# Performance work log

Measured on AMD Instinct MI355X. Metric: run time of the kernel, lower is better.

## Reference

```python
import jax, jax.numpy as jnp
import numpy as np

RATE = 0.2  # sparsification keep-rate from forward: sparse(x, 0.2)


def sparse_mask(x, rate):
    # Per-sample top-k over flattened NxN adjacency, scatter a 0/1 mask, multiply.
    b, n, _ = x.shape
    k = int(n * n * rate)
    flat = x.reshape(b, -1)
    _, idx = jax.lax.top_k(flat, k)  # [b, k]
    mask = jnp.zeros_like(flat).at[jnp.arange(b)[:, None], idx].set(1.0)
    return x * mask.reshape(b, n, n)


def gcn_layer(X, A, W, b):
    # Dense-batched equivalent of PyG GCNConv on dense_to_sparse(A) edges:
    # add self-loops (weight 1), symmetric-normalize by weighted degree,
    # aggregate source->target (row->col) messages of X @ W.
    n = A.shape[-1]
    Ah = A + jnp.eye(n, dtype=A.dtype)          # [B,N,N]
    deg = Ah.sum(axis=-2)                        # weighted in-degree (col sum), [B,N]
    dinv = jnp.where(deg > 0, 1.0 / jnp.sqrt(deg), 0.0)
    An = dinv[:, :, None] * Ah * dinv[:, None, :]  # norm_ij = d_i^-1/2 A_ij d_j^-1/2
    XW = X @ W                                     # [B,N,H]
    # out_j = sum_i An_ij * XW_i  (message flows row i -> col j)
    return jnp.einsum('bij,bih->bjh', An, XW) + b


def setup_inputs() -> dict:
    key = jax.random.key(0)
    ks = jax.random.split(key, 6)
    B, N, H = 1024, 200, 128
    return {
        "x": jax.random.uniform(ks[0], (B, N, N), jnp.float32),
        "adj": jax.random.uniform(ks[1], (B, N, N), jnp.float32),
        "W1": jax.random.normal(ks[2], (N, H), jnp.float32) * 0.05,
        "b1": jnp.zeros((H,), jnp.float32),
        "W2": jax.random.normal(ks[3], (H, H), jnp.float32) * 0.05,
        "b2": jnp.zeros((H,), jnp.float32),
    }


def reference(x, adj, W1, b1, W2, b2):
    # NOTE: the original forward immediately overwrites `adj` with sparse(x, 0.2).
    A = sparse_mask(x, RATE)
    h = jax.nn.relu(gcn_layer(x, A, W1, b1))  # GCNConv(200,128) + ReLU
    h = gcn_layer(h, A, W2, b2)                # GCNConv(128,128)
    return h.mean(axis=-2)                     # mean over nodes -> [B, 128]
```

## Files before the change

kernel.cpp:

```cpp
#include <hip/hip_runtime.h>

#define NB 1024
#define NNODE 200
#define NN2 40000
#define HD 128
#define KTOP 8000
#define NCH 7
#define NJT 13
#define XBS 232
#define A2S 40

#define WLO_BITS 0x3F47AE14u
#define WHI_BITS 0x3F51EB85u
#define CCAP 3072
#define C2CAP 64

typedef __attribute__((ext_vector_type(8))) short short8;
typedef __attribute__((ext_vector_type(4))) float f32x4;

__device__ __forceinline__ unsigned short f2bf(float f) {
  unsigned u = __float_as_uint(f);
  u = u + 0x7FFFu + ((u >> 16) & 1u);
  return (unsigned short)(u >> 16);
}

__device__ __forceinline__ float maskv(float v, int idx, unsigned vt, int it) {
  unsigned b = __float_as_uint(v);
  return (b > vt || (b == vt && idx <= it)) ? v : 0.0f;
}

__global__ void k_weights(const float* __restrict__ W1, unsigned short* __restrict__ wf) {
  int t = blockIdx.x * 256 + threadIdx.x;
  if (t >= NCH * 8 * 64) return;
  int lane = t & 63;
  int ht = (t >> 6) & 7;
  int ks = t >> 9;
  int c = lane & 15, q = lane >> 4;
  int h = ht * 16 + c;
  unsigned short v[8];
#pragma unroll
  for (int j = 0; j < 8; ++j) {
    int k = ks * 32 + q * 8 + j;
    v[j] = f2bf((k < NNODE) ? W1[k * HD + h] : 0.0f);
  }
  uint4 u;
  u.x = (unsigned)v[0] | ((unsigned)v[1] << 16);
  u.y = (unsigned)v[2] | ((unsigned)v[3] << 16);
  u.z = (unsigned)v[4] | ((unsigned)v[5] << 16);
  u.w = (unsigned)v[6] | ((unsigned)v[7] << 16);
  ((uint4*)wf)[t] = u;
}

__global__ __launch_bounds__(512) void k_prep(const float* __restrict__ x,
                                              unsigned* __restrict__ vtit,
                                              float* __restrict__ dinv_g) {
  __shared__ union {
    struct { unsigned cb[CCAP]; int ci[CCAP]; } w;
    unsigned hist[4096];
  } u;
  __shared__ unsigned sub[1024];
  __shared__ unsigned csum[512];
  __shared__ float degf[NNODE];
  __shared__ unsigned c2b[C2CAP];
  __shared__ int c2i[C2CAP];
  __shared__ int sc[4];
  __shared__ int cnt, cnt2, nhi_s, fbflag;
  __shared__ unsigned svt;
  __shared__ int sit;

  const int s = blockIdx.x, tid = threadIdx.x;
  const float* xp = x + (size_t)s * NN2;
  const float4* xp4 = (const float4*)xp;

  if (tid < NNODE) degf[tid] = 0.0f;
  if (tid == 0) { cnt = 0; cnt2 = 0; nhi_s = 0; fbflag = 0; }
  __syncthreads();

  int nhi = 0;
  for (int e = tid; e < NN2 / 4; e += 512) {
    float4 f = xp4[e];
    int base = e * 4;
    float vv[4] = {f.x, f.y, f.z, f.w};
#pragma unroll
    for (int k = 0; k < 4; ++k) {
      unsigned bits = __float_as_uint(vv[k]);
      if (bits > WHI_BITS) {
        atomicAdd(&degf[(base + k) % NNODE], vv[k]);
        ++nhi;
      } else if (bits >= WLO_BITS) {
        int p = atomicAdd(&cnt, 1);
        if (p < CCAP) { u.w.cb[p] = bits; u.w.ci[p] = base + k; }
      }
    }
  }
#pragma unroll
  for (int m = 1; m < 64; m <<= 1) nhi += __shfl_xor(nhi, m);
  if ((tid & 63) == 0) atomicAdd(&nhi_s, nhi);
  __syncthreads();

  const int need = KTOP - nhi_s;
  const int c = cnt;
  bool window_ok = (need >= 1) && (c <= CCAP) && (need <= c);

  if (window_ok) {
    for (int e = tid; e < 1024; e += 512) sub[e] = 0u;
    __syncthreads();
    for (int t = tid; t < c; t += 512) atomicAdd(&sub[(u.w.cb[t] >> 12) & 1023u], 1u);
    __syncthreads();
    if (tid < 128) {
      unsigned ss = 0;
#pragma unroll
      for (int k = 0; k < 8; ++k) ss += sub[tid * 8 + k];
      csum[tid] = ss;
    }
    __syncthreads();
    if (tid == 0) {
      int cum = 0, b2 = 0, need2 = need;
      for (int t = 127; t >= 0; --t) {
        int cs = (int)csum[t];
        if (cum + cs >= need) {
          for (int b = t * 8 + 7; b >= t * 8; --b) {
            int hb = (int)sub[b];
            if (cum + hb >= need) { b2 = b; need2 = need - cum; break; }
            cum += hb;
          }
          break;
        }
        cum += cs;
      }
      sc[0] = b2;
      sc[1] = need2;
    }
    __syncthreads();
    const unsigned b2 = (unsigned)sc[0];
    const int need2 = sc[1];
    for (int t = tid; t < c; t += 512) {
      if (((u.w.cb[t] >> 12) & 1023u) == b2) {
        int p = atomicAdd(&cnt2, 1);
        if (p < C2CAP) { c2b[p] = u.w.cb[t]; c2i[p] = u.w.ci[t]; }
      }
    }
    __syncthreads();
    if (cnt2 > C2CAP) {
      if (tid == 0) fbflag = 1;
    } else {
      const int c2 = cnt2;
      for (int t = tid; t < c2; t += 512) {
        unsigned vb = c2b[t];
        int vi = c2i[t];
        int rank = 0;
        for (int uu = 0; uu < c2; ++uu) {
          unsigned ub = c2b[uu];
          if (ub > vb || (ub == vb && c2i[uu] < vi)) ++rank;
        }
        if (rank == need2 - 1) { svt = vb; sit = vi; }
      }
    }
    __syncthreads();
    if (!fbflag) {
      const unsigned vt = svt;
      const int itx = sit;
      for (int t = tid; t < c; t += 512) {
        unsigned bits = u.w.cb[t];
        int e = u.w.ci[t];
        if (bits > vt || (bits == vt && e <= itx))
          atomicAdd(&degf[e % NNODE], __uint_as_float(bits));
      }
    }
  } else {
    if (tid == 0) fbflag = 1;
    __syncthreads();
  }
  __syncthreads();

  if (fbflag) {
    if (tid < NNODE) degf[tid] = 0.0f;
    for (int e = tid; e < 4096; e += 512) u.hist[e] = 0u;
    if (tid == 0) { cnt = 0; cnt2 = 0; }
    __syncthreads();
    for (int e = tid; e < NN2 / 4; e += 512) {
      float4 f = xp4[e];
      atomicAdd(&u.hist[__float_as_uint(f.x) >> 18], 1u);
      atomicAdd(&u.hist[__float_as_uint(f.y) >> 18], 1u);
      atomicAdd(&u.hist[__float_as_uint(f.z) >> 18], 1u);
      atomicAdd(&u.hist[__float_as_uint(f.w) >> 18], 1u);
    }
    __syncthreads();
    {
      unsigned ss = 0;
#pragma unroll
      for (int k = 0; k < 8; ++k) ss += u.hist[tid * 8 + k];
      csum[tid] = ss;
    }
    __syncthreads();
    if (tid == 0) {
      int cum = 0, bsel = 0, nd = KTOP;
      for (int t = 511; t >= 0; --t) {
        int cs = (int)csum[t];
        if (cum + cs >= KTOP) {
          for (int b = t * 8 + 7; b >= t * 8; --b) {
            int hb = (int)u.hist[b];
            if (cum + hb >= KTOP) { bsel = b; nd = KTOP - cum; break; }
            cum += hb;
          }
          break;
        }
        cum += cs;
      }
      sc[0] = bsel;
      sc[1] = nd;
    }
    __syncthreads();
    const int bsel = sc[0], nd = sc[1];
    for (int e = tid; e < NN2 / 4; e += 512) {
      float4 f = xp4[e];
      int base = e * 4;
      float vv[4] = {f.x, f.y, f.z, f.w};
#pragma unroll
      for (int k = 0; k < 4; ++k) {
        unsigned bits = __float_as_uint(vv[k]);
        int bk = (int)(bits >> 18);
        if (bk > bsel) {
          atomicAdd(&degf[(base + k) % NNODE], vv[k]);
        } else if (bk == bsel) {
          int p = atomicAdd(&cnt, 1);
          if (p < CCAP) { u.w.cb[p] = bits; u.w.ci[p] = base + k; }
        }
      }
    }
    for (int e = tid; e < 1024; e += 512) sub[e] = 0u;
    __syncthreads();
    const int cc = cnt < CCAP ? cnt : CCAP;
    for (int t = tid; t < cc; t += 512) atomicAdd(&sub[(u.w.cb[t] >> 8) & 1023u], 1u);
    __syncthreads();
    if (tid < 128) {
      unsigned ss = 0;
#pragma unroll
      for (int k = 0; k < 8; ++k) ss += sub[tid * 8 + k];
      csum[tid] = ss;
    }
    __syncthreads();
    if (tid == 0) {
      int cum = 0, b2 = 0, need2 = nd;
      for (int t = 127; t >= 0; --t) {
        int cs = (int)csum[t];
        if (cum + cs >= nd) {
          for (int b = t * 8 + 7; b >= t * 8; --b) {
            int hb = (int)sub[b];
            if (cum + hb >= nd) { b2 = b; need2 = nd - cum; break; }
            cum += hb;
          }
          break;
        }
        cum += cs;
      }
      sc[2] = b2;
      sc[3] = need2;
    }
    __syncthreads();
    const unsigned key = ((unsigned)bsel << 10) | (unsigned)sc[2];
    const int need2 = sc[3];
    for (int t = tid; t < cc; t += 512) {
      if ((u.w.cb[t] >> 8) == key) {
        int p = atomicAdd(&cnt2, 1);
        if (p < C2CAP) { c2b[p] = u.w.cb[t]; c2i[p] = u.w.ci[t]; }
      }
    }
    __syncthreads();
    {
      int c2 = cnt2 < C2CAP ? cnt2 : C2CAP;
      for (int t = tid; t < c2; t += 512) {
        unsigned vb = c2b[t];
        int vi = c2i[t];
        int rank = 0;
        for (int uu = 0; uu < c2; ++uu) {
          unsigned ub = c2b[uu];
          if (ub > vb || (ub == vb && c2i[uu] < vi)) ++rank;
        }
        if (rank == need2 - 1) { svt = vb; sit = vi; }
      }
    }
    __syncthreads();
    const unsigned vt = svt;
    const int itx = sit;
    for (int t = tid; t < cc; t += 512) {
      unsigned bits = u.w.cb[t];
      int e = u.w.ci[t];
      if (bits > vt || (bits == vt && e <= itx))
        atomicAdd(&degf[e % NNODE], __uint_as_float(bits));
    }
    __syncthreads();
  }

  if (tid < NNODE) dinv_g[s * NNODE + tid] = 1.0f / sqrtf(1.0f + degf[tid]);
  if (tid == 0) {
    vtit[s * 2 + 0] = svt;
    vtit[s * 2 + 1] = (unsigned)sit;
  }
}

__global__ __launch_bounds__(512, 4) void k_main(
    const float* __restrict__ x, const unsigned short* __restrict__ wf,
    const float* __restrict__ b1, const float* __restrict__ W2,
    const float* __restrict__ b2, const unsigned* __restrict__ vtit,
    const float* __restrict__ dinv_g, float* __restrict__ out) {
  __shared__ unsigned short xb[2][32][XBS];
  __shared__ unsigned short a2t[2][208][A2S];
  __shared__ float rowsum[224];
  __shared__ float dinv_l[224];
  __shared__ float gs[HD];
  __shared__ float pt[4][HD];

  const int s = blockIdx.x;
  const int tid = threadIdx.x;
  const int lane = tid & 63;
  const int w = tid >> 6;
  const int c = lane & 15;
  const int q = lane >> 4;
  const float* xp = x + (size_t)s * NN2;

  if (tid < 224) {
    dinv_l[tid] = (tid < NNODE) ? dinv_g[s * NNODE + tid] : 0.0f;
    rowsum[tid] = 0.0f;
  }
  const unsigned vt = vtit[s * 2];
  const int itx = (int)vtit[s * 2 + 1];

  const short8* bp = (const short8*)wf;
  short8 bfr[NCH];
#pragma unroll
  for (int ks = 0; ks < NCH; ++ks) bfr[ks] = bp[(ks * 8 + w) * 64 + lane];

  f32x4 acc2[NJT];
#pragma unroll
  for (int jt = 0; jt < NJT; ++jt) acc2[jt] = (f32x4){0.f, 0.f, 0.f, 0.f};

  auto stage = [&](int ic, int b) {
    const int r = tid >> 4, c0 = tid & 15;
    const int gi = ic * 32 + r;
    const bool rowok = gi < NNODE;
    const float di = dinv_l[gi];
    const int rb = gi * NNODE;
    float rs = 0.0f;
#pragma unroll
    for (int itc = 0; itc < 13; ++itc) {
      int col = c0 + itc * 16;
      unsigned short xbv = 0, a2v = 0;
      if (col < NNODE) {
        float v = rowok ? xp[rb + col] : 0.0f;
        xbv = f2bf(v);
        float am = maskv(v, rb + col, vt, itx);
        rs += am * dinv_l[col];
        if (gi == col) am += 1.0f;
        a2v = f2bf(am * di);
      }
      xb[b][r][col] = xbv;
      a2t[b][col][r] = a2v;
    }
    xb[b][r][208 + c0] = 0;
    atomicAdd(&rowsum[gi], rs);
  };

  __syncthreads();
  stage(0, 0);
  __syncthreads();

  for (int ic = 0; ic < NCH; ++ic) {
    const int cur = ic & 1;
    if (ic + 1 < NCH) stage(ic + 1, cur ^ 1);
    f32x4 a0 = (f32x4){0.f, 0.f, 0.f, 0.f}, a1 = (f32x4){0.f, 0.f, 0.f, 0.f};
#pragma unroll
    for (int ks = 0; ks < NCH; ++ks) {
      short8 af0 = *(const short8*)&xb[cur][c][ks * 32 + q * 8];
      short8 af1 = *(const short8*)&xb[cur][16 + c][ks * 32 + q * 8];
      a0 = __builtin_amdgcn_mfma_f32_16x16x32_bf16(af0, bfr[ks], a0, 0, 0, 0);
      a1 = __builtin_amdgcn_mfma_f32_16x16x32_bf16(af1, bfr[ks], a1, 0, 0, 0);
    }
    unsigned pk0[2], pk1[2];
    pk0[0] = (unsigned)f2bf(a0[0]) | ((unsigned)f2bf(a0[1]) << 16);
    pk0[1] = (unsigned)f2bf(a0[2]) | ((unsigned)f2bf(a0[3]) << 16);
    pk1[0] = (unsigned)f2bf(a1[0]) | ((unsigned)f2bf(a1[1]) << 16);
    pk1[1] = (unsigned)f2bf(a1[2]) | ((unsigned)f2bf(a1[3]) << 16);
    union {
      unsigned u[4];
      short8 s8;
    } ub;
#pragma unroll
    for (int d = 0; d < 4; ++d) {
      int src = c + (((q & 1) * 2 + (d >> 1)) << 4);
      unsigned lo = (unsigned)__shfl((int)pk0[d & 1], src);
      unsigned hi = (unsigned)__shfl((int)pk1[d & 1], src);
      ub.u[d] = (q >= 2) ? hi : lo;
    }
    short8 bf2 = ub.s8;
#pragma unroll
    for (int jt = 0; jt < NJT; ++jt) {
      short8 af = *(const short8*)&a2t[cur][jt * 16 + c][q * 8];
      acc2[jt] = __builtin_amdgcn_mfma_f32_16x16x32_bf16(af, bf2, acc2[jt], 0, 0, 0);
    }
    __syncthreads();
  }

  {
    const float bb = b1[w * 16 + c];
    float gp = 0.0f;
#pragma unroll
    for (int jt = 0; jt < NJT; ++jt) {
#pragma unroll
      for (int rg = 0; rg < 4; ++rg) {
        int j = jt * 16 + q * 4 + rg;
        if (j < NNODE) {
          float dj = dinv_l[j];
          float rj = dj * (rowsum[j] + dj);
          float o = fmaxf(dj * acc2[jt][rg] + bb, 0.0f);
          gp += rj * o;
        }
      }
    }
    gp += __shfl_xor(gp, 16);
    gp += __shfl_xor(gp, 32);
    if (q == 0) gs[w * 16 + c] = gp;
  }
  __syncthreads();
  {
    int h = tid & 127, seg = tid >> 7;
    float a = 0.0f;
#pragma unroll 8
    for (int cc = seg * 32; cc < seg * 32 + 32; ++cc) a += gs[cc] * W2[cc * HD + h];
    pt[seg][h] = a;
  }
  __syncthreads();
  if (tid < HD) {
    float a = pt[0][tid] + pt[1][tid] + pt[2][tid] + pt[3][tid];
    out[(size_t)s * HD + tid] = a * (1.0f / (float)NNODE) + b2[tid];
  }
}

extern "C" void kernel_launch(void* const* d_in, const int* in_sizes, int n_in,
                              void* d_out, int out_size, void* d_ws, size_t ws_size,
                              hipStream_t stream) {
  (void)in_sizes; (void)n_in; (void)out_size; (void)ws_size;
  const float* x = (const float*)d_in[0];
  const float* W1 = (const float*)d_in[2];
  const float* b1 = (const float*)d_in[3];
  const float* W2 = (const float*)d_in[4];
  const float* b2 = (const float*)d_in[5];
  float* out = (float*)d_out;

  unsigned short* wf = (unsigned short*)d_ws;
  unsigned* vtit = (unsigned*)((char*)d_ws + 57344);
  float* dinv_g = (float*)((char*)d_ws + 65536);

  k_weights<<<dim3(14), dim3(256), 0, stream>>>(W1, wf);
  k_prep<<<dim3(NB), dim3(512), 0, stream>>>(x, vtit, dinv_g);
  k_main<<<dim3(NB), dim3(512), 0, stream>>>(x, wf, b1, W2, b2, vtit, dinv_g, out);
}
```

Before: 439.1 us.

## Fuse weight prep, top-k threshold, and GCN main kernel into one launch

Merges the three kernels (W1 bf16 packing, per-sample top-k threshold/degree computation, and the MFMA GCN pass) into a single kernel that overlays their shared-memory buffers in a union. Each block now builds its W1 fragments directly from global memory and keeps the threshold and dinv values in shared memory rather than round-tripping them through workspace. The staging of x rows is split into register-prefetched halves interleaved with the MFMA work, and per-row rowsum is reduced with shuffles before a single atomic. It trades the launch gaps and intermediate traffic for redundant W1 conversion in every block and higher register pressure under launch_bounds(512,4).

```diff
diff --git a/kernel.cpp b/kernel.cpp
--- a/kernel.cpp
+++ b/kernel.cpp
@@ -29,50 +29,45 @@
   return (b > vt || (b == vt && idx <= it)) ? v : 0.0f;
 }
 
-__global__ void k_weights(const float* __restrict__ W1, unsigned short* __restrict__ wf) {
-  int t = blockIdx.x * 256 + threadIdx.x;
-  if (t >= NCH * 8 * 64) return;
-  int lane = t & 63;
-  int ht = (t >> 6) & 7;
-  int ks = t >> 9;
-  int c = lane & 15, q = lane >> 4;
-  int h = ht * 16 + c;
-  unsigned short v[8];
-#pragma unroll
-  for (int j = 0; j < 8; ++j) {
-    int k = ks * 32 + q * 8 + j;
-    v[j] = f2bf((k < NNODE) ? W1[k * HD + h] : 0.0f);
-  }
-  uint4 u;
-  u.x = (unsigned)v[0] | ((unsigned)v[1] << 16);
-  u.y = (unsigned)v[2] | ((unsigned)v[3] << 16);
-  u.z = (unsigned)v[4] | ((unsigned)v[5] << 16);
-  u.w = (unsigned)v[6] | ((unsigned)v[7] << 16);
-  ((uint4*)wf)[t] = u;
-}
-
-__global__ __launch_bounds__(512) void k_prep(const float* __restrict__ x,
-                                              unsigned* __restrict__ vtit,
-                                              float* __restrict__ dinv_g) {
+__global__ __launch_bounds__(512, 4) void k_fused(
+    const float* __restrict__ x, const float* __restrict__ W1,
+    const float* __restrict__ b1, const float* __restrict__ W2,
+    const float* __restrict__ b2, float* __restrict__ out) {
   __shared__ union {
-    struct { unsigned cb[CCAP]; int ci[CCAP]; } w;
-    unsigned hist[4096];
-  } u;
-  __shared__ unsigned sub[1024];
-  __shared__ unsigned csum[512];
-  __shared__ float degf[NNODE];
-  __shared__ unsigned c2b[C2CAP];
-  __shared__ int c2i[C2CAP];
+    struct {
+      union {
+        struct { unsigned cb[CCAP]; int ci[CCAP]; } w;
+        unsigned hist[4096];
+      } u;
+      unsigned sub[1024];
+      unsigned csum[512];
+      float degf[NNODE];
+      unsigned c2b[C2CAP];
+      int c2i[C2CAP];
+    } p;
+    struct {
+      unsigned short xb[2][32][XBS];
+      unsigned short a2t[2][208][A2S];
+    } m;
+  } S;
+  __shared__ float rowsum[224];
+  __shared__ float dinv_l[224];
+  __shared__ float gs[HD];
+  __shared__ float pt[4][HD];
   __shared__ int sc[4];
   __shared__ int cnt, cnt2, nhi_s, fbflag;
   __shared__ unsigned svt;
   __shared__ int sit;
 
   const int s = blockIdx.x, tid = threadIdx.x;
+  const int lane = tid & 63;
+  const int w = tid >> 6;
+  const int c = lane & 15;
+  const int q = lane >> 4;
   const float* xp = x + (size_t)s * NN2;
   const float4* xp4 = (const float4*)xp;
 
-  if (tid < NNODE) degf[tid] = 0.0f;
+  if (tid < NNODE) S.p.degf[tid] = 0.0f;
   if (tid == 0) { cnt = 0; cnt2 = 0; nhi_s = 0; fbflag = 0; }
   __syncthreads();
 
@@ -85,11 +80,11 @@
     for (int k = 0; k < 4; ++k) {
       unsigned bits = __float_as_uint(vv[k]);
       if (bits > WHI_BITS) {
-        atomicAdd(&degf[(base + k) % NNODE], vv[k]);
+        atomicAdd(&S.p.degf[(base + k) % NNODE], vv[k]);
         ++nhi;
       } else if (bits >= WLO_BITS) {
         int p = atomicAdd(&cnt, 1);
-        if (p < CCAP) { u.w.cb[p] = bits; u.w.ci[p] = base + k; }
+        if (p < CCAP) { S.p.u.w.cb[p] = bits; S.p.u.w.ci[p] = base + k; }
       }
     }
   }
@@ -99,28 +94,29 @@
   __syncthreads();
 
   const int need = KTOP - nhi_s;
-  const int c = cnt;
-  bool window_ok = (need >= 1) && (c <= CCAP) && (need <= c);
+  const int ccount = cnt;
+  bool window_ok = (need >= 1) && (ccount <= CCAP) && (need <= ccount);
 
   if (window_ok) {
-    for (int e = tid; e < 1024; e += 512) sub[e] = 0u;
-    __syncthreads();
-    for (int t = tid; t < c; t += 512) atomicAdd(&sub[(u.w.cb[t] >> 12) & 1023u], 1u);
+    for (int e = tid; e < 1024; e += 512) S.p.sub[e] = 0u;
+    __syncthreads();
+    for (int t = tid; t < ccount; t += 512)
+      atomicAdd(&S.p.sub[(S.p.u.w.cb[t] >> 12) & 1023u], 1u);
     __syncthreads();
     if (tid < 128) {
       unsigned ss = 0;
 #pragma unroll
-      for (int k = 0; k < 8; ++k) ss += sub[tid * 8 + k];
-      csum[tid] = ss;
+      for (int k = 0; k < 8; ++k) ss += S.p.sub[tid * 8 + k];
+      S.p.csum[tid] = ss;
     }
     __syncthreads();
     if (tid == 0) {
       int cum = 0, b2 = 0, need2 = need;
       for (int t = 127; t >= 0; --t) {
-        int cs = (int)csum[t];
+        int cs = (int)S.p.csum[t];
         if (cum + cs >= need) {
           for (int b = t * 8 + 7; b >= t * 8; --b) {
-            int hb = (int)sub[b];
+            int hb = (int)S.p.sub[b];
             if (cum + hb >= need) { b2 = b; need2 = need - cum; break; }
             cum += hb;
           }
@@ -134,10 +130,10 @@
     __syncthreads();
     const unsigned b2 = (unsigned)sc[0];
     const int need2 = sc[1];
-    for (int t = tid; t < c; t += 512) {
-      if (((u.w.cb[t] >> 12) & 1023u) == b2) {
+    for (int t = tid; t < ccount; t += 512) {
+      if (((S.p.u.w.cb[t] >> 12) & 1023u) == b2) {
         int p = atomicAdd(&cnt2, 1);
-        if (p < C2CAP) { c2b[p] = u.w.cb[t]; c2i[p] = u.w.ci[t]; }
+        if (p < C2CAP) { S.p.c2b[p] = S.p.u.w.cb[t]; S.p.c2i[p] = S.p.u.w.ci[t]; }
       }
     }
     __syncthreads();
@@ -146,25 +142,25 @@
     } else {
       const int c2 = cnt2;
       for (int t = tid; t < c2; t += 512) {
-        unsigned vb = c2b[t];
-        int vi = c2i[t];
+        unsigned vb = S.p.c2b[t];
+        int vi = S.p.c2i[t];
         int rank = 0;
         for (int uu = 0; uu < c2; ++uu) {
-          unsigned ub = c2b[uu];
-          if (ub > vb || (ub == vb && c2i[uu] < vi)) ++rank;
+          unsigned ub = S.p.c2b[uu];
+          if (ub > vb || (ub == vb && S.p.c2i[uu] < vi)) ++rank;
         }
         if (rank == need2 - 1) { svt = vb; sit = vi; }
       }
     }
     __syncthreads();
     if (!fbflag) {
-      const unsigned vt = svt;
-      const int itx = sit;
-      for (int t = tid; t < c; t += 512) {
-        unsigned bits = u.w.cb[t];
-        int e = u.w.ci[t];
-        if (bits > vt || (bits == vt && e <= itx))
-          atomicAdd(&degf[e % NNODE], __uint_as_float(bits));
+      const unsigned vt0 = svt;
+      const int itx0 = sit;
+      for (int t = tid; t < ccount; t += 512) {
+        unsigned bits = S.p.u.w.cb[t];
+        int e = S.p.u.w.ci[t];
+        if (bits > vt0 || (bits == vt0 && e <= itx0))
+          atomicAdd(&S.p.degf[e % NNODE], __uint_as_float(bits));
       }
     }
   } else {
@@ -174,32 +170,32 @@
   __syncthreads();
 
   if (fbflag) {
-    if (tid < NNODE) degf[tid] = 0.0f;
-    for (int e = tid; e < 4096; e += 512) u.hist[e] = 0u;
+    if (tid < NNODE) S.p.degf[tid] = 0.0f;
+    for (int e = tid; e < 4096; e += 512) S.p.u.hist[e] = 0u;
     if (tid == 0) { cnt = 0; cnt2 = 0; }
     __syncthreads();
     for (int e = tid; e < NN2 / 4; e += 512) {
       float4 f = xp4[e];
-      atomicAdd(&u.hist[__float_as_uint(f.x) >> 18], 1u);
-      atomicAdd(&u.hist[__float_as_uint(f.y) >> 18], 1u);
-      atomicAdd(&u.hist[__float_as_uint(f.z) >> 18], 1u);
-      atomicAdd(&u.hist[__float_as_uint(f.w) >> 18], 1u);
+      atomicAdd(&S.p.u.hist[__float_as_uint(f.x) >> 18], 1u);
+      atomicAdd(&S.p.u.hist[__float_as_uint(f.y) >> 18], 1u);
+      atomicAdd(&S.p.u.hist[__float_as_uint(f.z) >> 18], 1u);
+      atomicAdd(&S.p.u.hist[__float_as_uint(f.w) >> 18], 1u);
     }
     __syncthreads();
     {
       unsigned ss = 0;
 #pragma unroll
-      for (int k = 0; k < 8; ++k) ss += u.hist[tid * 8 + k];
-      csum[tid] = ss;
+      for (int k = 0; k < 8; ++k) ss += S.p.u.hist[tid * 8 + k];
+      S.p.csum[tid] = ss;
     }
     __syncthreads();
     if (tid == 0) {
       int cum = 0, bsel = 0, nd = KTOP;
       for (int t = 511; t >= 0; --t) {
-        int cs = (int)csum[t];
+        int cs = (int)S.p.csum[t];
         if (cum + cs >= KTOP) {
           for (int b = t * 8 + 7; b >= t * 8; --b) {
-            int hb = (int)u.hist[b];
+            int hb = (int)S.p.u.hist[b];
             if (cum + hb >= KTOP) { bsel = b; nd = KTOP - cum; break; }
             cum += hb;
           }
@@ -221,32 +217,33 @@
         unsigned bits = __float_as_uint(vv[k]);
         int bk = (int)(bits >> 18);
         if (bk > bsel) {
-          atomicAdd(&degf[(base + k) % NNODE], vv[k]);
+          atomicAdd(&S.p.degf[(base + k) % NNODE], vv[k]);
         } else if (bk == bsel) {
           int p = atomicAdd(&cnt, 1);
-          if (p < CCAP) { u.w.cb[p] = bits; u.w.ci[p] = base + k; }
-        }
-      }
-    }
-    for (int e = tid; e < 1024; e += 512) sub[e] = 0u;
+          if (p < CCAP) { S.p.u.w.cb[p] = bits; S.p.u.w.ci[p] = base + k; }
+        }
+      }
+    }
+    for (int e = tid; e < 1024; e += 512) S.p.sub[e] = 0u;
     __syncthreads();
     const int cc = cnt < CCAP ? cnt : CCAP;
-    for (int t = tid; t < cc; t += 512) atomicAdd(&sub[(u.w.cb[t] >> 8) & 1023u], 1u);
+    for (int t = tid; t < cc; t += 512)
+      atomicAdd(&S.p.sub[(S.p.u.w.cb[t] >> 8) & 1023u], 1u);
     __syncthreads();
     if (tid < 128) {
       unsigned ss = 0;
 #pragma unroll
-      for (int k = 0; k < 8; ++k) ss += sub[tid * 8 + k];
-      csum[tid] = ss;
+      for (int k = 0; k < 8; ++k) ss += S.p.sub[tid * 8 + k];
+      S.p.csum[tid] = ss;
     }
     __syncthreads();
     if (tid == 0) {
       int cum = 0, b2 = 0, need2 = nd;
       for (int t = 127; t >= 0; --t) {
-        int cs = (int)csum[t];
+        int cs = (int)S.p.csum[t];
         if (cum + cs >= nd) {
           for (int b = t * 8 + 7; b >= t * 8; --b) {
-            int hb = (int)sub[b];
+            int hb = (int)S.p.sub[b];
             if (cum + hb >= nd) { b2 = b; need2 = nd - cum; break; }
             cum += hb;
           }
@@ -261,120 +258,157 @@
     const unsigned key = ((unsigned)bsel << 10) | (unsigned)sc[2];
     const int need2 = sc[3];
     for (int t = tid; t < cc; t += 512) {
-      if ((u.w.cb[t] >> 8) == key) {
+      if ((S.p.u.w.cb[t] >> 8) == key) {
         int p = atomicAdd(&cnt2, 1);
-        if (p < C2CAP) { c2b[p] = u.w.cb[t]; c2i[p] = u.w.ci[t]; }
+        if (p < C2CAP) { S.p.c2b[p] = S.p.u.w.cb[t]; S.p.c2i[p] = S.p.u.w.ci[t]; }
       }
     }
     __syncthreads();
     {
       int c2 = cnt2 < C2CAP ? cnt2 : C2CAP;
       for (int t = tid; t < c2; t += 512) {
-        unsigned vb = c2b[t];
-        int vi = c2i[t];
+        unsigned vb = S.p.c2b[t];
+        int vi = S.p.c2i[t];
         int rank = 0;
         for (int uu = 0; uu < c2; ++uu) {
-          unsigned ub = c2b[uu];
-          if (ub > vb || (ub == vb && c2i[uu] < vi)) ++rank;
+          unsigned ub = S.p.c2b[uu];
+          if (ub > vb || (ub == vb && S.p.c2i[uu] < vi)) ++rank;
         }
         if (rank == need2 - 1) { svt = vb; sit = vi; }
       }
     }
     __syncthreads();
-    const unsigned vt = svt;
-    const int itx = sit;
+    const unsigned vt1 = svt;
+    const int itx1 = sit;
     for (int t = tid; t < cc; t += 512) {
-      unsigned bits = u.w.cb[t];
-      int e = u.w.ci[t];
-      if (bits > vt || (bits == vt && e <= itx))
-        atomicAdd(&degf[e % NNODE], __uint_as_float(bits));
-    }
-    __syncthreads();
-  }
-
-  if (tid < NNODE) dinv_g[s * NNODE + tid] = 1.0f / sqrtf(1.0f + degf[tid]);
-  if (tid == 0) {
-    vtit[s * 2 + 0] = svt;
-    vtit[s * 2 + 1] = (unsigned)sit;
-  }
-}
-
-__global__ __launch_bounds__(512, 4) void k_main(
-    const float* __restrict__ x, const unsigned short* __restrict__ wf,
-    const float* __restrict__ b1, const float* __restrict__ W2,
-    const float* __restrict__ b2, const unsigned* __restrict__ vtit,
-    const float* __restrict__ dinv_g, float* __restrict__ out) {
-  __shared__ unsigned short xb[2][32][XBS];
-  __shared__ unsigned short a2t[2][208][A2S];
-  __shared__ float rowsum[224];
-  __shared__ float dinv_l[224];
-  __shared__ float gs[HD];
-  __shared__ float pt[4][HD];
-
-  const int s = blockIdx.x;
-  const int tid = threadIdx.x;
-  const int lane = tid & 63;
-  const int w = tid >> 6;
-  const int c = lane & 15;
-  const int q = lane >> 4;
-  const float* xp = x + (size_t)s * NN2;
+      unsigned bits = S.p.u.w.cb[t];
+      int e = S.p.u.w.ci[t];
+      if (bits > vt1 || (bits == vt1 && e <= itx1))
+        atomicAdd(&S.p.degf[e % NNODE], __uint_as_float(bits));
+    }
+    __syncthreads();
+  }
 
   if (tid < 224) {
-    dinv_l[tid] = (tid < NNODE) ? dinv_g[s * NNODE + tid] : 0.0f;
+    dinv_l[tid] = (tid < NNODE) ? (1.0f / sqrtf(1.0f + S.p.degf[tid])) : 0.0f;
     rowsum[tid] = 0.0f;
   }
-  const unsigned vt = vtit[s * 2];
-  const int itx = (int)vtit[s * 2 + 1];
-
-  const short8* bp = (const short8*)wf;
+  const unsigned vt = svt;
+  const int itx = sit;
+
   short8 bfr[NCH];
 #pragma unroll
-  for (int ks = 0; ks < NCH; ++ks) bfr[ks] = bp[(ks * 8 + w) * 64 + lane];
+  for (int ks = 0; ks < NCH; ++ks) {
+    unsigned short vv[8];
+#pragma unroll
+    for (int j = 0; j < 8; ++j) {
+      int k = ks * 32 + q * 8 + j;
+      vv[j] = f2bf((k < NNODE) ? W1[k * HD + w * 16 + c] : 0.0f);
+    }
+    union { unsigned u4[4]; short8 s8; } pw;
+    pw.u4[0] = (unsigned)vv[0] | ((unsigned)vv[1] << 16);
+    pw.u4[1] = (unsigned)vv[2] | ((unsigned)vv[3] << 16);
+    pw.u4[2] = (unsigned)vv[4] | ((unsigned)vv[5] << 16);
+    pw.u4[3] = (unsigned)vv[6] | ((unsigned)vv[7] << 16);
+    bfr[ks] = pw.s8;
+  }
+  __syncthreads();
 
   f32x4 acc2[NJT];
 #pragma unroll
   for (int jt = 0; jt < NJT; ++jt) acc2[jt] = (f32x4){0.f, 0.f, 0.f, 0.f};
 
-  auto stage = [&](int ic, int b) {
-    const int r = tid >> 4, c0 = tid & 15;
-    const int gi = ic * 32 + r;
+  const int r_ = tid >> 4, c0_ = tid & 15;
+  float va[7], vb[6];
+
+  auto load_A = [&](int ic) {
+    const int gi = ic * 32 + r_;
     const bool rowok = gi < NNODE;
+    const int rb = gi * NNODE;
+#pragma unroll
+    for (int itc = 0; itc < 7; ++itc) {
+      int col = c0_ + itc * 16;
+      va[itc] = rowok ? xp[rb + col] : 0.0f;
+    }
+  };
+  auto load_B = [&](int ic) {
+    const int gi = ic * 32 + r_;
+    const bool rowok = gi < NNODE;
+    const int rb = gi * NNODE;
+#pragma unroll
+    for (int itc = 7; itc < 13; ++itc) {
+      int col = c0_ + itc * 16;
+      vb[itc - 7] = (rowok && col < NNODE) ? xp[rb + col] : 0.0f;
+    }
+  };
+  auto write_A = [&](int ic, int b, float& rs) {
+    const int gi = ic * 32 + r_;
     const float di = dinv_l[gi];
     const int rb = gi * NNODE;
-    float rs = 0.0f;
-#pragma unroll
-    for (int itc = 0; itc < 13; ++itc) {
-      int col = c0 + itc * 16;
+#pragma unroll
+    for (int itc = 0; itc < 7; ++itc) {
+      int col = c0_ + itc * 16;
+      float val = va[itc];
+      unsigned short xbv = f2bf(val);
+      float am = maskv(val, rb + col, vt, itx);
+      rs += am * dinv_l[col];
+      if (gi == col) am += 1.0f;
+      S.m.xb[b][r_][col] = xbv;
+      S.m.a2t[b][col][r_] = f2bf(am * di);
+    }
+  };
+  auto write_B = [&](int ic, int b, float& rs) {
+    const int gi = ic * 32 + r_;
+    const float di = dinv_l[gi];
+    const int rb = gi * NNODE;
+#pragma unroll
+    for (int itc = 7; itc < 13; ++itc) {
+      int col = c0_ + itc * 16;
       unsigned short xbv = 0, a2v = 0;
       if (col < NNODE) {
-        float v = rowok ? xp[rb + col] : 0.0f;
-        xbv = f2bf(v);
-        float am = maskv(v, rb + col, vt, itx);
+        float val = vb[itc - 7];
+        xbv = f2bf(val);
+        float am = maskv(val, rb + col, vt, itx);
         rs += am * dinv_l[col];
         if (gi == col) am += 1.0f;
         a2v = f2bf(am * di);
       }
-      xb[b][r][col] = xbv;
-      a2t[b][col][r] = a2v;
-    }
-    xb[b][r][208 + c0] = 0;
-    atomicAdd(&rowsum[gi], rs);
+      S.m.xb[b][r_][col] = xbv;
+      S.m.a2t[b][col][r_] = a2v;
+    }
+    S.m.xb[b][r_][208 + c0_] = 0;
+    rs += __shfl_xor(rs, 1);
+    rs += __shfl_xor(rs, 2);
+    rs += __shfl_xor(rs, 4);
+    rs += __shfl_xor(rs, 8);
+    if (c0_ == 0) atomicAdd(&rowsum[gi], rs);
   };
 
-  __syncthreads();
-  stage(0, 0);
+  load_A(0);
+  load_B(0);
+  {
+    float rs = 0.0f;
+    write_A(0, 0, rs);
+    write_B(0, 0, rs);
+  }
   __syncthreads();
 
   for (int ic = 0; ic < NCH; ++ic) {
     const int cur = ic & 1;
-    if (ic + 1 < NCH) stage(ic + 1, cur ^ 1);
+    const bool more = (ic + 1 < NCH);
+    if (more) load_A(ic + 1);
     f32x4 a0 = (f32x4){0.f, 0.f, 0.f, 0.f}, a1 = (f32x4){0.f, 0.f, 0.f, 0.f};
 #pragma unroll
     for (int ks = 0; ks < NCH; ++ks) {
-      short8 af0 = *(const short8*)&xb[cur][c][ks * 32 + q * 8];
-      short8 af1 = *(const short8*)&xb[cur][16 + c][ks * 32 + q * 8];
+      short8 af0 = *(const short8*)&S.m.xb[cur][c][ks * 32 + q * 8];
+      short8 af1 = *(const short8*)&S.m.xb[cur][16 + c][ks * 32 + q * 8];
       a0 = __builtin_amdgcn_mfma_f32_16x16x32_bf16(af0, bfr[ks], a0, 0, 0, 0);
       a1 = __builtin_amdgcn_mfma_f32_16x16x32_bf16(af1, bfr[ks], a1, 0, 0, 0);
+    }
+    float rs = 0.0f;
+    if (more) {
+      write_A(ic + 1, cur ^ 1, rs);
+      load_B(ic + 1);
     }
     unsigned pk0[2], pk1[2];
     pk0[0] = (unsigned)f2bf(a0[0]) | ((unsigned)f2bf(a0[1]) << 16);
@@ -382,7 +416,7 @@
     pk1[0] = (unsigned)f2bf(a1[0]) | ((unsigned)f2bf(a1[1]) << 16);
     pk1[1] = (unsigned)f2bf(a1[2]) | ((unsigned)f2bf(a1[3]) << 16);
     union {
-      unsigned u[4];
+      unsigned u4[4];
       short8 s8;
     } ub;
 #pragma unroll
@@ -390,14 +424,15 @@
       int src = c + (((q & 1) * 2 + (d >> 1)) << 4);
       unsigned lo = (unsigned)__shfl((int)pk0[d & 1], src);
       unsigned hi = (unsigned)__shfl((int)pk1[d & 1], src);
-      ub.u[d] = (q >= 2) ? hi : lo;
+      ub.u4[d] = (q >= 2) ? hi : lo;
     }
     short8 bf2 = ub.s8;
 #pragma unroll
     for (int jt = 0; jt < NJT; ++jt) {
-      short8 af = *(const short8*)&a2t[cur][jt * 16 + c][q * 8];
+      short8 af = *(const short8*)&S.m.a2t[cur][jt * 16 + c][q * 8];
       acc2[jt] = __builtin_amdgcn_mfma_f32_16x16x32_bf16(af, bf2, acc2[jt], 0, 0, 0);
     }
+    if (more) write_B(ic + 1, cur ^ 1, rs);
     __syncthreads();
   }
 
@@ -426,7 +461,7 @@
     int h = tid & 127, seg = tid >> 7;
     float a = 0.0f;
 #pragma unroll 8
-    for (int cc = seg * 32; cc < seg * 32 + 32; ++cc) a += gs[cc] * W2[cc * HD + h];
+    for (int cc2 = seg * 32; cc2 < seg * 32 + 32; ++cc2) a += gs[cc2] * W2[cc2 * HD + h];
     pt[seg][h] = a;
   }
   __syncthreads();
@@ -439,7 +474,7 @@
 extern "C" void kernel_launch(void* const* d_in, const int* in_sizes, int n_in,
                               void* d_out, int out_size, void* d_ws, size_t ws_size,
                               hipStream_t stream) {
-  (void)in_sizes; (void)n_in; (void)out_size; (void)ws_size;
+  (void)in_sizes; (void)n_in; (void)out_size; (void)d_ws; (void)ws_size;
   const float* x = (const float*)d_in[0];
   const float* W1 = (const float*)d_in[2];
   const float* b1 = (const float*)d_in[3];
@@ -447,11 +482,5 @@
   const float* b2 = (const float*)d_in[5];
   float* out = (float*)d_out;
 
-  unsigned short* wf = (unsigned short*)d_ws;
-  unsigned* vtit = (unsigned*)((char*)d_ws + 57344);
-  float* dinv_g = (float*)((char*)d_ws + 65536);
-
-  k_weights<<<dim3(14), dim3(256), 0, stream>>>(W1, wf);
-  k_prep<<<dim3(NB), dim3(512), 0, stream>>>(x, vtit, dinv_g);
-  k_main<<<dim3(NB), dim3(512), 0, stream>>>(x, wf, b1, W2, b2, vtit, dinv_g, out);
+  k_fused<<<dim3(NB), dim3(512), 0, stream>>>(x, W1, b1, W2, b2, out);
 }
```

Result: slower. 464.2 us (+5.7%).

## Software-pipeline x staging loads with MFMA compute and fold W1 conversion into main kernel

Applied to the files above, without the earlier changes.

Splits the per-chunk staging into register loads issued before the MFMA work and LDS writes interleaved after each MFMA phase, so global load latency overlaps tensor-core compute. It also drops the separate W1 bf16 pre-pack kernel and has each block convert W1 fragments directly from global memory. Row-sum accumulation now goes through a wave shuffle reduction with one LDS atomic per row instead of one per thread. The trade-offs are higher register pressure from holding the prefetched values, and every block redundantly reading and converting W1 with strided loads.

```diff
diff --git a/kernel.cpp b/kernel.cpp
--- a/kernel.cpp
+++ b/kernel.cpp
@@ -27,28 +27,6 @@
 __device__ __forceinline__ float maskv(float v, int idx, unsigned vt, int it) {
   unsigned b = __float_as_uint(v);
   return (b > vt || (b == vt && idx <= it)) ? v : 0.0f;
-}
-
-__global__ void k_weights(const float* __restrict__ W1, unsigned short* __restrict__ wf) {
-  int t = blockIdx.x * 256 + threadIdx.x;
-  if (t >= NCH * 8 * 64) return;
-  int lane = t & 63;
-  int ht = (t >> 6) & 7;
-  int ks = t >> 9;
-  int c = lane & 15, q = lane >> 4;
-  int h = ht * 16 + c;
-  unsigned short v[8];
-#pragma unroll
-  for (int j = 0; j < 8; ++j) {
-    int k = ks * 32 + q * 8 + j;
-    v[j] = f2bf((k < NNODE) ? W1[k * HD + h] : 0.0f);
-  }
-  uint4 u;
-  u.x = (unsigned)v[0] | ((unsigned)v[1] << 16);
-  u.y = (unsigned)v[2] | ((unsigned)v[3] << 16);
-  u.z = (unsigned)v[4] | ((unsigned)v[5] << 16);
-  u.w = (unsigned)v[6] | ((unsigned)v[7] << 16);
-  ((uint4*)wf)[t] = u;
 }
 
 __global__ __launch_bounds__(512) void k_prep(const float* __restrict__ x,
@@ -299,8 +277,76 @@
   }
 }
 
+#define STAGE_LOAD_A(ic_)                                              \
+  {                                                                    \
+    const int gi = (ic_)*32 + r_;                                      \
+    const bool rowok = gi < NNODE;                                     \
+    const int rb = gi * NNODE;                                         \
+    _Pragma("unroll") for (int itc = 0; itc < 7; ++itc) {              \
+      int col = c0_ + itc * 16;               \
+      va[itc] = rowok ? xp[rb + col] : 0.0f;                           \
+    }                                                                  \
+  }
+
+#define STAGE_LOAD_B(ic_)                                              \
+  {                                                                    \
+    const int gi = (ic_)*32 + r_;                                      \
+    const bool rowok = gi < NNODE;                                     \
+    const int rb = gi * NNODE;                                         \
+    _Pragma("unroll") for (int itc = 7; itc < 13; ++itc) {             \
+      int col = c0_ + itc * 16;                                        \
+      vb[itc - 7] = (rowok && col < NNODE) ? xp[rb + col] : 0.0f;      \
+    }                                                                  \
+  }
+
+#define STAGE_WRITE_A(ic_, bb_)                                        \
+  {                                                                    \
+    const int gi = (ic_)*32 + r_;                                      \
+    const float di = dinv_l[gi];                                       \
+    const int rb = gi * NNODE;                                         \
+    rsA = 0.0f;                                                        \
+    _Pragma("unroll") for (int itc = 0; itc < 7; ++itc) {              \
+      int col = c0_ + itc * 16;                                        \
+      float val = va[itc];                                             \
+      unsigned short xbv = f2bf(val);                                  \
+      float am = maskv(val, rb + col, vt, itx);                        \
+      rsA += am * dinv_l[col];                                         \
+      if (gi == col) am += 1.0f;                                       \
+      xb[bb_][r_][col] = xbv;                                          \
+      a2t[bb_][col][r_] = f2bf(am * di);                               \
+    }                                                                  \
+  }
+
+#define STAGE_WRITE_B(ic_, bb_)                                        \
+  {                                                                    \
+    const int gi = (ic_)*32 + r_;                                      \
+    const float di = dinv_l[gi];                                       \
+    const int rb = gi * NNODE;                                         \
+    float rs = rsA;                                                    \
+    _Pragma("unroll") for (int itc = 7; itc < 13; ++itc) {             \
+      int col = c0_ + itc * 16;                                        \
+      unsigned short xbv = 0, a2v = 0;                                 \
+      if (col < NNODE) {                                               \
+        float val = vb[itc - 7];                                       \
+        xbv = f2bf(val);                                               \
+        float am = maskv(val, rb + col, vt, itx);                      \
+        rs += am * dinv_l[col];                                        \
+        if (gi == col) am += 1.0f;                                     \
+        a2v = f2bf(am * di);                                           \
+      }                                                                \
+      xb[bb_][r_][col] = xbv;                                          \
+      a2t[bb_][col][r_] = a2v;                                         \
+    }                                                                  \
+    xb[bb_][r_][208 + c0_] = 0;                    \
+    rs += __shfl_xor(rs, 1);                                           \
+    rs += __shfl_xor(rs, 2);                                           \
+    rs += __shfl_xor(rs, 4);                                           \
+    rs += __shfl_xor(rs, 8);                                           \
+    if (c0_ == 0) atomicAdd(&rowsum[gi], rs);                          \
+  }
+
 __global__ __launch_bounds__(512, 4) void k_main(
-    const float* __restrict__ x, const unsigned short* __restrict__ wf,
+    const float* __restrict__ x, const float* __restrict__ W1,
     const float* __restrict__ b1, const float* __restrict__ W2,
     const float* __restrict__ b2, const unsigned* __restrict__ vtit,
     const float* __restrict__ dinv_g, float* __restrict__ out) {
@@ -325,49 +371,46 @@
   }
   const unsigned vt = vtit[s * 2];
   const int itx = (int)vtit[s * 2 + 1];
-
-  const short8* bp = (const short8*)wf;
+  const int r_ = tid >> 4, c0_ = tid & 15;
+
+  float va[7], vb[6], rsA;
+
+  STAGE_LOAD_A(0);
+  STAGE_LOAD_B(0);
+
   short8 bfr[NCH];
 #pragma unroll
-  for (int ks = 0; ks < NCH; ++ks) bfr[ks] = bp[(ks * 8 + w) * 64 + lane];
+  for (int ks = 0; ks < NCH; ++ks) {
+    unsigned short vv[8];
+#pragma unroll
+    for (int j = 0; j < 8; ++j) {
+      int k = ks * 32 + q * 8 + j;
+      vv[j] = f2bf((k < NNODE) ? W1[k * HD + w * 16 + c] : 0.0f);
+    }
+    union { unsigned u4[4]; short8 s8; } pw;
+    pw.u4[0] = (unsigned)vv[0] | ((unsigned)vv[1] << 16);
+    pw.u4[1] = (unsigned)vv[2] | ((unsigned)vv[3] << 16);
+    pw.u4[2] = (unsigned)vv[4] | ((unsigned)vv[5] << 16);
+    pw.u4[3] = (unsigned)vv[6] | ((unsigned)vv[7] << 16);
+    bfr[ks] = pw.s8;
+  }
 
   f32x4 acc2[NJT];
 #pragma unroll
   for (int jt = 0; jt < NJT; ++jt) acc2[jt] = (f32x4){0.f, 0.f, 0.f, 0.f};
 
-  auto stage = [&](int ic, int b) {
-    const int r = tid >> 4, c0 = tid & 15;
-    const int gi = ic * 32 + r;
-    const bool rowok = gi < NNODE;
-    const float di = dinv_l[gi];
-    const int rb = gi * NNODE;
-    float rs = 0.0f;
-#pragma unroll
-    for (int itc = 0; itc < 13; ++itc) {
-      int col = c0 + itc * 16;
-      unsigned short xbv = 0, a2v = 0;
-      if (col < NNODE) {
-        float v = rowok ? xp[rb + col] : 0.0f;
-        xbv = f2bf(v);
-        float am = maskv(v, rb + col, vt, itx);
-        rs += am * dinv_l[col];
-        if (gi == col) am += 1.0f;
-        a2v = f2bf(am * di);
-      }
-      xb[b][r][col] = xbv;
-      a2t[b][col][r] = a2v;
-    }
-    xb[b][r][208 + c0] = 0;
-    atomicAdd(&rowsum[gi], rs);
-  };
-
-  __syncthreads();
-  stage(0, 0);
+  __syncthreads();
+  STAGE_WRITE_A(0, 0);
+  STAGE_WRITE_B(0, 0);
   __syncthreads();
 
   for (int ic = 0; ic < NCH; ++ic) {
     const int cur = ic & 1;
-    if (ic + 1 < NCH) stage(ic + 1, cur ^ 1);
+    const bool more = (ic + 1 < NCH);
+    if (more) {
+      STAGE_LOAD_A(ic + 1);
+      STAGE_LOAD_B(ic + 1);
+    }
     f32x4 a0 = (f32x4){0.f, 0.f, 0.f, 0.f}, a1 = (f32x4){0.f, 0.f, 0.f, 0.f};
 #pragma unroll
     for (int ks = 0; ks < NCH; ++ks) {
@@ -376,13 +419,14 @@
       a0 = __builtin_amdgcn_mfma_f32_16x16x32_bf16(af0, bfr[ks], a0, 0, 0, 0);
       a1 = __builtin_amdgcn_mfma_f32_16x16x32_bf16(af1, bfr[ks], a1, 0, 0, 0);
     }
+    if (more) STAGE_WRITE_A(ic + 1, cur ^ 1);
     unsigned pk0[2], pk1[2];
     pk0[0] = (unsigned)f2bf(a0[0]) | ((unsigned)f2bf(a0[1]) << 16);
     pk0[1] = (unsigned)f2bf(a0[2]) | ((unsigned)f2bf(a0[3]) << 16);
     pk1[0] = (unsigned)f2bf(a1[0]) | ((unsigned)f2bf(a1[1]) << 16);
     pk1[1] = (unsigned)f2bf(a1[2]) | ((unsigned)f2bf(a1[3]) << 16);
     union {
-      unsigned u[4];
+      unsigned u4[4];
       short8 s8;
     } ub;
 #pragma unroll
@@ -390,7 +434,7 @@
       int src = c + (((q & 1) * 2 + (d >> 1)) << 4);
       unsigned lo = (unsigned)__shfl((int)pk0[d & 1], src);
       unsigned hi = (unsigned)__shfl((int)pk1[d & 1], src);
-      ub.u[d] = (q >= 2) ? hi : lo;
+      ub.u4[d] = (q >= 2) ? hi : lo;
     }
     short8 bf2 = ub.s8;
 #pragma unroll
@@ -398,6 +442,7 @@
       short8 af = *(const short8*)&a2t[cur][jt * 16 + c][q * 8];
       acc2[jt] = __builtin_amdgcn_mfma_f32_16x16x32_bf16(af, bf2, acc2[jt], 0, 0, 0);
     }
+    if (more) STAGE_WRITE_B(ic + 1, cur ^ 1);
     __syncthreads();
   }
 
@@ -447,11 +492,9 @@
   const float* b2 = (const float*)d_in[5];
   float* out = (float*)d_out;
 
-  unsigned short* wf = (unsigned short*)d_ws;
-  unsigned* vtit = (unsigned*)((char*)d_ws + 57344);
-  float* dinv_g = (float*)((char*)d_ws + 65536);
-
-  k_weights<<<dim3(14), dim3(256), 0, stream>>>(W1, wf);
+  unsigned* vtit = (unsigned*)d_ws;
+  float* dinv_g = (float*)((char*)d_ws + 8192);
+
   k_prep<<<dim3(NB), dim3(512), 0, stream>>>(x, vtit, dinv_g);
-  k_main<<<dim3(NB), dim3(512), 0, stream>>>(x, wf, b1, W2, b2, vtit, dinv_g, out);
+  k_main<<<dim3(NB), dim3(512), 0, stream>>>(x, W1, b1, W2, b2, vtit, dinv_g, out);
 }
```

After: 408.8 us. 6.9% less time.

## Split staging into early global loads and late LDS writes with float2 vectors

Applied to the files above, without the earlier changes.

The staging of the next chunk is split so its global loads are issued before the MFMA work and its conversion and LDS writes happen afterwards, which hides load latency behind compute. Each thread now loads contiguous float2 pairs instead of strided scalars. Row sums are reduced with wave shuffles before a single atomic per row. The W1 fragments are reloaded from global memory every iteration instead of being held in registers, which lowers register pressure but adds repeated loads. The top-k scan loop is also unrolled.

```diff
diff --git a/kernel.cpp b/kernel.cpp
--- a/kernel.cpp
+++ b/kernel.cpp
@@ -22,6 +22,10 @@
   unsigned u = __float_as_uint(f);
   u = u + 0x7FFFu + ((u >> 16) & 1u);
   return (unsigned short)(u >> 16);
+}
+
+__device__ __forceinline__ unsigned pack2bf(float lo, float hi) {
+  return (unsigned)f2bf(lo) | ((unsigned)f2bf(hi) << 16);
 }
 
 __device__ __forceinline__ float maskv(float v, int idx, unsigned vt, int it) {
@@ -77,6 +81,7 @@
   __syncthreads();
 
   int nhi = 0;
+#pragma unroll 4
   for (int e = tid; e < NN2 / 4; e += 512) {
     float4 f = xp4[e];
     int base = e * 4;
@@ -299,6 +304,76 @@
   }
 }
 
+#define STAGE_LOAD_A(ic_)                                               \
+  {                                                                     \
+    const int gi = (ic_)*32 + r_;                                       \
+    const bool rowok = gi < NNODE;                                      \
+    const int rb = gi * NNODE;                                          \
+    _Pragma("unroll") for (int k = 0; k < 4; ++k) {                     \
+      int col0 = k * 32 + 2 * c0_;                           \
+      va[k] = rowok ? *(const float2*)&xp[rb + col0]                    \
+                    : (float2){0.0f, 0.0f};                             \
+    }                                                                   \
+  }
+
+#define STAGE_LOAD_B(ic_)                                               \
+  {                                                                     \
+    const int gi = (ic_)*32 + r_;                                       \
+    const bool rowok = gi < NNODE;                                      \
+    const int rb = gi * NNODE;                                          \
+    _Pragma("unroll") for (int k = 4; k < 6; ++k) {                     \
+      int col0 = k * 32 + 2 * c0_;                           \
+      vb[k - 4] = rowok ? *(const float2*)&xp[rb + col0]                \
+                        : (float2){0.0f, 0.0f};                         \
+    }                                                                   \
+    vb[2] = (rowok && c0_ < 4) ? *(const float2*)&xp[rb + 192 + 2 * c0_]\
+                               : (float2){0.0f, 0.0f};                  \
+  }
+
+#define PAIR_BODY(v0_, v1_, col0_, bb_)                                 \
+  {                                                                     \
+    *(unsigned*)&xb[bb_][r_][col0_] = pack2bf(v0_, v1_);                \
+    float am0 = maskv(v0_, rb + col0_, vt, itx);                        \
+    float am1 = maskv(v1_, rb + col0_ + 1, vt, itx);                    \
+    rs += am0 * dinv_l[col0_] + am1 * dinv_l[col0_ + 1];                \
+    if (gi == col0_) am0 += 1.0f;                                       \
+    if (gi == col0_ + 1) am1 += 1.0f;                                   \
+    if (col0_ < 208) {                                                  \
+      a2t[bb_][col0_][r_] = f2bf(am0 * di);                             \
+      a2t[bb_][col0_ + 1][r_] = f2bf(am1 * di);                         \
+    }                                                                   \
+  }
+
+#define STAGE_WRITE_A(ic_, bb_)                                         \
+  {                                                                     \
+    const int gi = (ic_)*32 + r_;                                       \
+    const float di = dinv_l[gi];                                        \
+    const int rb = gi * NNODE;                                          \
+    float rs = 0.0f;                                                    \
+    _Pragma("unroll") for (int k = 0; k < 4; ++k) {                     \
+      int col0 = k * 32 + 2 * c0_;                                      \
+      PAIR_BODY(va[k].x, va[k].y, col0, bb_);                           \
+    }                                                                   \
+    rsA = rs;                                                           \
+  }
+
+#define STAGE_WRITE_B(ic_, bb_)                                         \
+  {                                                                     \
+    const int gi = (ic_)*32 + r_;                                       \
+    const float di = dinv_l[gi];                                        \
+    const int rb = gi * NNODE;                                          \
+    float rs = rsA;                                                     \
+    _Pragma("unroll") for (int k = 4; k < 7; ++k) {                     \
+      int col0 = k * 32 + 2 * c0_;                                      \
+      PAIR_BODY(vb[k - 4].x, vb[k - 4].y, col0, bb_);                   \
+    }                                                                   \
+    rs += __shfl_xor(rs, 1);                                            \
+    rs += __shfl_xor(rs, 2);                                            \
+    rs += __shfl_xor(rs, 4);                                            \
+    rs += __shfl_xor(rs, 8);                                            \
+    if (c0_ == 0) atomicAdd(&rowsum[gi], rs);                           \
+  }
+
 __global__ __launch_bounds__(512, 4) void k_main(
     const float* __restrict__ x, const unsigned short* __restrict__ wf,
     const float* __restrict__ b1, const float* __restrict__ W2,
@@ -318,6 +393,7 @@
   const int c = lane & 15;
   const int q = lane >> 4;
   const float* xp = x + (size_t)s * NN2;
+  const short8* wfp = (const short8*)wf;
 
   if (tid < 224) {
     dinv_l[tid] = (tid < NNODE) ? dinv_g[s * NNODE + tid] : 0.0f;
@@ -325,64 +401,48 @@
   }
   const unsigned vt = vtit[s * 2];
   const int itx = (int)vtit[s * 2 + 1];
-
-  const short8* bp = (const short8*)wf;
-  short8 bfr[NCH];
-#pragma unroll
-  for (int ks = 0; ks < NCH; ++ks) bfr[ks] = bp[(ks * 8 + w) * 64 + lane];
+  const int r_ = tid >> 4, c0_ = tid & 15;
+
+  float2 va[4], vb[3];
+  float rsA;
+
+  STAGE_LOAD_A(0);
+  STAGE_LOAD_B(0);
 
   f32x4 acc2[NJT];
 #pragma unroll
   for (int jt = 0; jt < NJT; ++jt) acc2[jt] = (f32x4){0.f, 0.f, 0.f, 0.f};
 
-  auto stage = [&](int ic, int b) {
-    const int r = tid >> 4, c0 = tid & 15;
-    const int gi = ic * 32 + r;
-    const bool rowok = gi < NNODE;
-    const float di = dinv_l[gi];
-    const int rb = gi * NNODE;
-    float rs = 0.0f;
-#pragma unroll
-    for (int itc = 0; itc < 13; ++itc) {
-      int col = c0 + itc * 16;
-      unsigned short xbv = 0, a2v = 0;
-      if (col < NNODE) {
-        float v = rowok ? xp[rb + col] : 0.0f;
-        xbv = f2bf(v);
-        float am = maskv(v, rb + col, vt, itx);
-        rs += am * dinv_l[col];
-        if (gi == col) am += 1.0f;
-        a2v = f2bf(am * di);
-      }
-      xb[b][r][col] = xbv;
-      a2t[b][col][r] = a2v;
-    }
-    xb[b][r][208 + c0] = 0;
-    atomicAdd(&rowsum[gi], rs);
-  };
-
-  __syncthreads();
-  stage(0, 0);
+  __syncthreads();
+  STAGE_WRITE_A(0, 0);
+  STAGE_WRITE_B(0, 0);
   __syncthreads();
 
   for (int ic = 0; ic < NCH; ++ic) {
     const int cur = ic & 1;
-    if (ic + 1 < NCH) stage(ic + 1, cur ^ 1);
+    const bool more = (ic + 1 < NCH);
+    short8 wfr[NCH];
+#pragma unroll
+    for (int ks = 0; ks < NCH; ++ks) wfr[ks] = wfp[(ks * 8 + w) * 64 + lane];
+    if (more) {
+      STAGE_LOAD_A(ic + 1);
+      STAGE_LOAD_B(ic + 1);
+    }
     f32x4 a0 = (f32x4){0.f, 0.f, 0.f, 0.f}, a1 = (f32x4){0.f, 0.f, 0.f, 0.f};
 #pragma unroll
     for (int ks = 0; ks < NCH; ++ks) {
       short8 af0 = *(const short8*)&xb[cur][c][ks * 32 + q * 8];
       short8 af1 = *(const short8*)&xb[cur][16 + c][ks * 32 + q * 8];
-      a0 = __builtin_amdgcn_mfma_f32_16x16x32_bf16(af0, bfr[ks], a0, 0, 0, 0);
-      a1 = __builtin_amdgcn_mfma_f32_16x16x32_bf16(af1, bfr[ks], a1, 0, 0, 0);
+      a0 = __builtin_amdgcn_mfma_f32_16x16x32_bf16(af0, wfr[ks], a0, 0, 0, 0);
+      a1 = __builtin_amdgcn_mfma_f32_16x16x32_bf16(af1, wfr[ks], a1, 0, 0, 0);
     }
     unsigned pk0[2], pk1[2];
-    pk0[0] = (unsigned)f2bf(a0[0]) | ((unsigned)f2bf(a0[1]) << 16);
-    pk0[1] = (unsigned)f2bf(a0[2]) | ((unsigned)f2bf(a0[3]) << 16);
-    pk1[0] = (unsigned)f2bf(a1[0]) | ((unsigned)f2bf(a1[1]) << 16);
-    pk1[1] = (unsigned)f2bf(a1[2]) | ((unsigned)f2bf(a1[3]) << 16);
+    pk0[0] = pack2bf(a0[0], a0[1]);
+    pk0[1] = pack2bf(a0[2], a0[3]);
+    pk1[0] = pack2bf(a1[0], a1[1]);
+    pk1[1] = pack2bf(a1[2], a1[3]);
     union {
-      unsigned u[4];
+      unsigned u4[4];
       short8 s8;
     } ub;
 #pragma unroll
@@ -390,13 +450,17 @@
       int src = c + (((q & 1) * 2 + (d >> 1)) << 4);
       unsigned lo = (unsigned)__shfl((int)pk0[d & 1], src);
       unsigned hi = (unsigned)__shfl((int)pk1[d & 1], src);
-      ub.u[d] = (q >= 2) ? hi : lo;
+      ub.u4[d] = (q >= 2) ? hi : lo;
     }
     short8 bf2 = ub.s8;
 #pragma unroll
     for (int jt = 0; jt < NJT; ++jt) {
       short8 af = *(const short8*)&a2t[cur][jt * 16 + c][q * 8];
       acc2[jt] = __builtin_amdgcn_mfma_f32_16x16x32_bf16(af, bf2, acc2[jt], 0, 0, 0);
+    }
+    if (more) {
+      STAGE_WRITE_A(ic + 1, cur ^ 1);
+      STAGE_WRITE_B(ic + 1, cur ^ 1);
     }
     __syncthreads();
   }
```

Result: faster. 413.5 us (-5.8%).
